# Kernel optimization log

Measured on AMD Instinct MI355X. Metric: run time of the kernel, lower is better.

## Reference

```python
import jax, jax.numpy as jnp
import numpy as np

M, K, N = 8192, 4096, 4096

def setup_inputs() -> dict:
    key = jax.random.key(0)
    k1, k2, k3, k4 = jax.random.split(key, 4)
    x = jax.random.normal(k1, (M, K), dtype=jnp.float32)
    # pre-quantized int8 weights [K, N] and per-output-channel scales [N]
    weight_q = jax.random.randint(k2, (K, N), -128, 128, dtype=jnp.int32).astype(jnp.int8)
    weight_scale = (jax.random.uniform(k3, (N,), dtype=jnp.float32) * 0.01 + 1e-4)
    bias = jax.random.normal(k4, (N,), dtype=jnp.float32) * 0.02
    return {"x": x, "weight_q": weight_q, "weight_scale": weight_scale, "bias": bias}

def reference(x, weight_q, weight_scale, bias):
    # dynamic per-row int8 quantization of activations
    max_vals = jnp.max(jnp.abs(x), axis=-1, keepdims=True)          # [M, 1]
    a_scale = jnp.maximum(max_vals / 127.0, 1e-8)                    # [M, 1]
    x_q = jnp.clip(jnp.round(x / a_scale), -128, 127).astype(jnp.int8)
    c = jnp.matmul(x_q.astype(jnp.float32), weight_q.astype(jnp.float32))  # [M, N]
    # dequantize: per-row activation scale * per-column weight scale
    c = c * a_scale * weight_scale[None, :]
    out = c.astype(x.dtype) + bias
    return out
```

## Files before the change

### kernel.cpp

```cpp
#include <hip/hip_runtime.h>


typedef int int32x4 __attribute__((ext_vector_type(4)));

#define TILE_BM 128
#define TILE_BN 128
#define TILE_BK 64

__device__ __forceinline__ void async_copy16(const void* g, void* l) {
    __builtin_amdgcn_global_load_lds(
        (const __attribute__((address_space(1))) unsigned int*)g,
        (__attribute__((address_space(3))) unsigned int*)l,
        16, 0, 0);
}

__device__ __forceinline__ int quant1(float x, float s) {
    float q = rintf(x / s);
    q = fminf(127.0f, fmaxf(-128.0f, q));
    return (int)q;
}

__global__ __launch_bounds__(256) void quant_kernel(
    const float* __restrict__ x, signed char* __restrict__ xq,
    float* __restrict__ ascale, int K)
{
    const int row = blockIdx.x;
    const int t = threadIdx.x;
    const float4* xr4 = (const float4*)(x + (size_t)row * K);

    float4 v[4];
    float mx = 0.0f;
#pragma unroll
    for (int i = 0; i < 4; ++i) {
        v[i] = xr4[t * 4 + i];
        mx = fmaxf(mx, fmaxf(fmaxf(fabsf(v[i].x), fabsf(v[i].y)),
                             fmaxf(fabsf(v[i].z), fabsf(v[i].w))));
    }
#pragma unroll
    for (int off = 32; off > 0; off >>= 1)
        mx = fmaxf(mx, __shfl_xor(mx, off, 64));
    __shared__ float wmax[4];
    if ((t & 63) == 0) wmax[t >> 6] = mx;
    __syncthreads();
    mx = fmaxf(fmaxf(wmax[0], wmax[1]), fmaxf(wmax[2], wmax[3]));

    const float s = fmaxf(mx / 127.0f, 1e-8f);
    if (t == 0) ascale[row] = s;

    int out[4];
#pragma unroll
    for (int i = 0; i < 4; ++i) {
        const int b0 = quant1(v[i].x, s);
        const int b1 = quant1(v[i].y, s);
        const int b2 = quant1(v[i].z, s);
        const int b3 = quant1(v[i].w, s);
        out[i] = (b0 & 255) | ((b1 & 255) << 8) | ((b2 & 255) << 16) | ((b3 & 255) << 24);
    }
    *(int32x4*)(xq + (size_t)row * K + t * 16) = *(const int32x4*)out;
}

__global__ __launch_bounds__(256) void transpose_pack_kernel(
    const int* __restrict__ Bq, signed char* __restrict__ Bt, int K, int N)
{
    __shared__ int lds[64 * 17];
    const int t = threadIdx.x;
    const int n0 = blockIdx.x * 64;
    const int k0 = blockIdx.y * 64;

    const int r = t >> 4;
    const int ncol = (t & 15) * 4;

    const int* src = Bq + (size_t)(k0 + 4 * r) * N + n0 + ncol;
    const int4 u0 = *(const int4*)(src);
    const int4 u1 = *(const int4*)(src + N);
    const int4 u2 = *(const int4*)(src + 2 * (size_t)N);
    const int4 u3 = *(const int4*)(src + 3 * (size_t)N);

    lds[(ncol + 0) * 17 + r] = (u0.x & 255) | ((u1.x & 255) << 8) | ((u2.x & 255) << 16) | ((u3.x & 255) << 24);
    lds[(ncol + 1) * 17 + r] = (u0.y & 255) | ((u1.y & 255) << 8) | ((u2.y & 255) << 16) | ((u3.y & 255) << 24);
    lds[(ncol + 2) * 17 + r] = (u0.z & 255) | ((u1.z & 255) << 8) | ((u2.z & 255) << 16) | ((u3.z & 255) << 24);
    lds[(ncol + 3) * 17 + r] = (u0.w & 255) | ((u1.w & 255) << 8) | ((u2.w & 255) << 16) | ((u3.w & 255) << 24);
    __syncthreads();

    const int nl = t >> 2, ch = t & 3;
    int o[4];
#pragma unroll
    for (int i = 0; i < 4; ++i) o[i] = lds[nl * 17 + ch * 4 + i];
    *(int32x4*)(Bt + (size_t)(n0 + nl) * K + k0 + ch * 16) = *(const int32x4*)o;
}

__global__ __launch_bounds__(256, 2) void gemm_i8_kernel(
    const signed char* __restrict__ Aq, const signed char* __restrict__ Bt,
    const float* __restrict__ ascale, const float* __restrict__ wscale,
    const float* __restrict__ bias, float* __restrict__ C,
    int M, int N, int K)
{
    __shared__ __align__(16) signed char As[TILE_BM * TILE_BK];
    __shared__ __align__(16) signed char Bs[TILE_BN * TILE_BK];

    const int t = threadIdx.x;
    const int lane = t & 63;
    const int w = t >> 6;
    const int wr = w >> 1, wc = w & 1;

    const int m0 = blockIdx.y * TILE_BM;
    const int n0 = blockIdx.x * TILE_BN;

    const int srow = t >> 2;
    const int schunk = (t & 3) * 16;
    const signed char* gA0 = Aq + (size_t)(m0 + srow) * K + schunk;
    const signed char* gA1 = gA0 + (size_t)64 * K;
    const signed char* gB0 = Bt + (size_t)(n0 + srow) * K + schunk;
    const signed char* gB1 = gB0 + (size_t)64 * K;
    signed char* lA0 = As + t * 16;
    signed char* lA1 = lA0 + 4096;
    signed char* lB0 = Bs + t * 16;
    signed char* lB1 = lB0 + 4096;

    const int kb16 = (lane >> 4) * 16;
    const int ml = lane & 15;
    const signed char* fA = As + (wr * 64 + ml) * TILE_BK + kb16;
    const signed char* fB = Bs + (wc * 64 + ml) * TILE_BK + kb16;

    int32x4 acc[4][4] = {};

    for (int k0 = 0; k0 < K; k0 += TILE_BK) {
        async_copy16(gA0 + k0, lA0);
        async_copy16(gA1 + k0, lA1);
        async_copy16(gB0 + k0, lB0);
        async_copy16(gB1 + k0, lB1);
        __syncthreads();

        int32x4 af[4], bf[4];
#pragma unroll
        for (int i = 0; i < 4; ++i) {
            af[i] = *(const int32x4*)(fA + i * 16 * TILE_BK);
            bf[i] = *(const int32x4*)(fB + i * 16 * TILE_BK);
        }
#pragma unroll
        for (int i = 0; i < 4; ++i)
#pragma unroll
            for (int j = 0; j < 4; ++j)
                acc[i][j] = __builtin_amdgcn_mfma_i32_16x16x64_i8(af[i], bf[j], acc[i][j], 0, 0, 0);
        __syncthreads();
    }

    const int colb = n0 + wc * 64 + ml;
    const int rowb = m0 + wr * 64 + (lane >> 4) * 4;
#pragma unroll
    for (int j = 0; j < 4; ++j) {
        const int col = colb + j * 16;
        const float ws = wscale[col];
        const float bs = bias[col];
#pragma unroll
        for (int i = 0; i < 4; ++i) {
            const int row = rowb + i * 16;
            float* cp = C + (size_t)row * N + col;
#pragma unroll
            for (int r = 0; r < 4; ++r) {
                cp[(size_t)r * N] = ((float)acc[i][j][r] * ascale[row + r]) * ws + bs;
            }
        }
    }
}

extern "C" void kernel_launch(void* const* d_in, const int* in_sizes, int n_in,
                              void* d_out, int out_size, void* d_ws, size_t ws_size,
                              hipStream_t stream) {
    const float* x      = (const float*)d_in[0];
    const int*   wq     = (const int*)d_in[1];
    const float* wscale = (const float*)d_in[2];
    const float* bias   = (const float*)d_in[3];
    float* out          = (float*)d_out;

    const int N = in_sizes[2];
    const int K = in_sizes[1] / N;
    const int M = in_sizes[0] / K;

    char* ws = (char*)d_ws;
    signed char* xq = (signed char*)ws;
    signed char* bt = (signed char*)(ws + (size_t)M * K);
    float* ascale   = (float*)(ws + (size_t)M * K + (size_t)N * K);

    quant_kernel<<<M, 256, 0, stream>>>(x, xq, ascale, K);
    transpose_pack_kernel<<<dim3(N / 64, K / 64), 256, 0, stream>>>(wq, bt, K, N);
    gemm_i8_kernel<<<dim3(N / TILE_BN, M / TILE_BM), 256, 0, stream>>>(
        xq, bt, ascale, wscale, bias, out, M, N, K);
}
```

Measured before the change: 427.5 us.

## Fuse prep kernels, switch GEMM to 32x32 MFMA with BK=128 and swizzled LDS

The quantization and weight transpose/pack kernels are merged into one launch whose blocks branch on index, which removes one launch and lets the two jobs overlap. The GEMM K-tile doubles to 128, the 16x16x64 int8 MFMA is replaced with 32x32x32 in a 2x2 per-wave layout, and an XOR swizzle is applied to LDS chunks to avoid bank conflicts. The goal is fewer barriers per K, fewer LDS fragment reads per MFMA, and a vectorized ascale load in the epilogue. LDS use doubles to 32KB per block while launch bounds ask for 3 blocks per CU, which could raise register pressure.

```diff
diff --git a/kernel.cpp b/kernel.cpp
--- a/kernel.cpp
+++ b/kernel.cpp
@@ -1,11 +1,13 @@
 #include <hip/hip_runtime.h>
 
 
-typedef int int32x4 __attribute__((ext_vector_type(4)));
+typedef int   int32x4  __attribute__((ext_vector_type(4)));
+typedef int   int32x16 __attribute__((ext_vector_type(16)));
+typedef float floatx4  __attribute__((ext_vector_type(4)));
 
-#define TILE_BM 128
-#define TILE_BN 128
-#define TILE_BK 64
+#define BM 128
+#define BN 128
+#define BK 128
 
 __device__ __forceinline__ void async_copy16(const void* g, void* l) {
     __builtin_amdgcn_global_load_lds(
@@ -20,145 +22,153 @@
     return (int)q;
 }
 
-__global__ __launch_bounds__(256) void quant_kernel(
-    const float* __restrict__ x, signed char* __restrict__ xq,
-    float* __restrict__ ascale, int K)
+__global__ __launch_bounds__(256) void prep_kernel(
+    const float* __restrict__ x, const int* __restrict__ Bq,
+    signed char* __restrict__ xq, signed char* __restrict__ Bt,
+    float* __restrict__ ascale, int M, int K, int N)
 {
-    const int row = blockIdx.x;
+    __shared__ __align__(16) int shmem[64 * 17];
     const int t = threadIdx.x;
-    const float4* xr4 = (const float4*)(x + (size_t)row * K);
+    const int b = (int)blockIdx.x;
 
-    float4 v[4];
-    float mx = 0.0f;
+    if (b < M) {
+        const int row = b;
+        const float4* xr4 = (const float4*)(x + (size_t)row * K);
+        float4 v[4];
+        float mx = 0.0f;
 #pragma unroll
-    for (int i = 0; i < 4; ++i) {
-        v[i] = xr4[t * 4 + i];
-        mx = fmaxf(mx, fmaxf(fmaxf(fabsf(v[i].x), fabsf(v[i].y)),
-                             fmaxf(fabsf(v[i].z), fabsf(v[i].w))));
+        for (int i = 0; i < 4; ++i) {
+            v[i] = xr4[t * 4 + i];
+            mx = fmaxf(mx, fmaxf(fmaxf(fabsf(v[i].x), fabsf(v[i].y)),
+                                 fmaxf(fabsf(v[i].z), fabsf(v[i].w))));
+        }
+#pragma unroll
+        for (int off = 32; off > 0; off >>= 1)
+            mx = fmaxf(mx, __shfl_xor(mx, off, 64));
+        float* wmax = (float*)shmem;
+        if ((t & 63) == 0) wmax[t >> 6] = mx;
+        __syncthreads();
+        mx = fmaxf(fmaxf(wmax[0], wmax[1]), fmaxf(wmax[2], wmax[3]));
+
+        const float s = fmaxf(mx / 127.0f, 1e-8f);
+        if (t == 0) ascale[row] = s;
+
+        int out[4];
+#pragma unroll
+        for (int i = 0; i < 4; ++i) {
+            const int b0 = quant1(v[i].x, s);
+            const int b1 = quant1(v[i].y, s);
+            const int b2 = quant1(v[i].z, s);
+            const int b3 = quant1(v[i].w, s);
+            out[i] = (b0 & 255) | ((b1 & 255) << 8) | ((b2 & 255) << 16) | ((b3 & 255) << 24);
+        }
+        *(int32x4*)(xq + (size_t)row * K + t * 16) = *(const int32x4*)out;
+    } else {
+        const int tile = b - M;
+        const int tiles_n = N >> 6;
+        const int n0 = (tile % tiles_n) * 64;
+        const int k0 = (tile / tiles_n) * 64;
+
+        const int r = t >> 4;
+        const int ncol = (t & 15) * 4;
+
+        const int* src = Bq + (size_t)(k0 + 4 * r) * N + n0 + ncol;
+        const int4 u0 = *(const int4*)(src);
+        const int4 u1 = *(const int4*)(src + N);
+        const int4 u2 = *(const int4*)(src + 2 * (size_t)N);
+        const int4 u3 = *(const int4*)(src + 3 * (size_t)N);
+
+        shmem[(ncol + 0) * 17 + r] = (u0.x & 255) | ((u1.x & 255) << 8) | ((u2.x & 255) << 16) | ((u3.x & 255) << 24);
+        shmem[(ncol + 1) * 17 + r] = (u0.y & 255) | ((u1.y & 255) << 8) | ((u2.y & 255) << 16) | ((u3.y & 255) << 24);
+        shmem[(ncol + 2) * 17 + r] = (u0.z & 255) | ((u1.z & 255) << 8) | ((u2.z & 255) << 16) | ((u3.z & 255) << 24);
+        shmem[(ncol + 3) * 17 + r] = (u0.w & 255) | ((u1.w & 255) << 8) | ((u2.w & 255) << 16) | ((u3.w & 255) << 24);
+        __syncthreads();
+
+        const int nl = t >> 2, ch = t & 3;
+        int o[4];
+#pragma unroll
+        for (int i = 0; i < 4; ++i) o[i] = shmem[nl * 17 + ch * 4 + i];
+        *(int32x4*)(Bt + (size_t)(n0 + nl) * K + k0 + ch * 16) = *(const int32x4*)o;
     }
-#pragma unroll
-    for (int off = 32; off > 0; off >>= 1)
-        mx = fmaxf(mx, __shfl_xor(mx, off, 64));
-    __shared__ float wmax[4];
-    if ((t & 63) == 0) wmax[t >> 6] = mx;
-    __syncthreads();
-    mx = fmaxf(fmaxf(wmax[0], wmax[1]), fmaxf(wmax[2], wmax[3]));
-
-    const float s = fmaxf(mx / 127.0f, 1e-8f);
-    if (t == 0) ascale[row] = s;
-
-    int out[4];
-#pragma unroll
-    for (int i = 0; i < 4; ++i) {
-        const int b0 = quant1(v[i].x, s);
-        const int b1 = quant1(v[i].y, s);
-        const int b2 = quant1(v[i].z, s);
-        const int b3 = quant1(v[i].w, s);
-        out[i] = (b0 & 255) | ((b1 & 255) << 8) | ((b2 & 255) << 16) | ((b3 & 255) << 24);
-    }
-    *(int32x4*)(xq + (size_t)row * K + t * 16) = *(const int32x4*)out;
 }
 
-__global__ __launch_bounds__(256) void transpose_pack_kernel(
-    const int* __restrict__ Bq, signed char* __restrict__ Bt, int K, int N)
-{
-    __shared__ int lds[64 * 17];
-    const int t = threadIdx.x;
-    const int n0 = blockIdx.x * 64;
-    const int k0 = blockIdx.y * 64;
-
-    const int r = t >> 4;
-    const int ncol = (t & 15) * 4;
-
-    const int* src = Bq + (size_t)(k0 + 4 * r) * N + n0 + ncol;
-    const int4 u0 = *(const int4*)(src);
-    const int4 u1 = *(const int4*)(src + N);
-    const int4 u2 = *(const int4*)(src + 2 * (size_t)N);
-    const int4 u3 = *(const int4*)(src + 3 * (size_t)N);
-
-    lds[(ncol + 0) * 17 + r] = (u0.x & 255) | ((u1.x & 255) << 8) | ((u2.x & 255) << 16) | ((u3.x & 255) << 24);
-    lds[(ncol + 1) * 17 + r] = (u0.y & 255) | ((u1.y & 255) << 8) | ((u2.y & 255) << 16) | ((u3.y & 255) << 24);
-    lds[(ncol + 2) * 17 + r] = (u0.z & 255) | ((u1.z & 255) << 8) | ((u2.z & 255) << 16) | ((u3.z & 255) << 24);
-    lds[(ncol + 3) * 17 + r] = (u0.w & 255) | ((u1.w & 255) << 8) | ((u2.w & 255) << 16) | ((u3.w & 255) << 24);
-    __syncthreads();
-
-    const int nl = t >> 2, ch = t & 3;
-    int o[4];
-#pragma unroll
-    for (int i = 0; i < 4; ++i) o[i] = lds[nl * 17 + ch * 4 + i];
-    *(int32x4*)(Bt + (size_t)(n0 + nl) * K + k0 + ch * 16) = *(const int32x4*)o;
-}
-
-__global__ __launch_bounds__(256, 2) void gemm_i8_kernel(
+__global__ __launch_bounds__(256, 3) void gemm_i8_kernel(
     const signed char* __restrict__ Aq, const signed char* __restrict__ Bt,
     const float* __restrict__ ascale, const float* __restrict__ wscale,
     const float* __restrict__ bias, float* __restrict__ C,
     int M, int N, int K)
 {
-    __shared__ __align__(16) signed char As[TILE_BM * TILE_BK];
-    __shared__ __align__(16) signed char Bs[TILE_BN * TILE_BK];
+    __shared__ __align__(16) signed char As[BM * BK];
+    __shared__ __align__(16) signed char Bs[BN * BK];
 
     const int t = threadIdx.x;
     const int lane = t & 63;
     const int w = t >> 6;
     const int wr = w >> 1, wc = w & 1;
 
-    const int m0 = blockIdx.y * TILE_BM;
-    const int n0 = blockIdx.x * TILE_BN;
+    const int m0 = blockIdx.y * BM;
+    const int n0 = blockIdx.x * BN;
 
-    const int srow = t >> 2;
-    const int schunk = (t & 3) * 16;
-    const signed char* gA0 = Aq + (size_t)(m0 + srow) * K + schunk;
-    const signed char* gA1 = gA0 + (size_t)64 * K;
-    const signed char* gB0 = Bt + (size_t)(n0 + srow) * K + schunk;
-    const signed char* gB1 = gB0 + (size_t)64 * K;
-    signed char* lA0 = As + t * 16;
-    signed char* lA1 = lA0 + 4096;
-    signed char* lB0 = Bs + t * 16;
-    signed char* lB1 = lB0 + 4096;
+    const int srow = t >> 3;
+    const int schunk = ((t & 7) ^ (srow & 7)) * 16;
+    const signed char* gA = Aq + (size_t)(m0 + srow) * K + schunk;
+    const signed char* gB = Bt + (size_t)(n0 + srow) * K + schunk;
+    signed char* lA = As + t * 16;
+    signed char* lB = Bs + t * 16;
 
-    const int kb16 = (lane >> 4) * 16;
-    const int ml = lane & 15;
-    const signed char* fA = As + (wr * 64 + ml) * TILE_BK + kb16;
-    const signed char* fB = Bs + (wc * 64 + ml) * TILE_BK + kb16;
+    const int ml = lane & 31;
+    const int half = lane >> 5;
+    const int sw = ml & 7;
+    const signed char* fA0 = As + (wr * 64 + ml) * BK;
+    const signed char* fA1 = fA0 + 32 * BK;
+    const signed char* fB0 = Bs + (wc * 64 + ml) * BK;
+    const signed char* fB1 = fB0 + 32 * BK;
 
-    int32x4 acc[4][4] = {};
+    int32x16 acc[2][2] = {};
 
-    for (int k0 = 0; k0 < K; k0 += TILE_BK) {
-        async_copy16(gA0 + k0, lA0);
-        async_copy16(gA1 + k0, lA1);
-        async_copy16(gB0 + k0, lB0);
-        async_copy16(gB1 + k0, lB1);
+    for (int k0 = 0; k0 < K; k0 += BK) {
+#pragma unroll
+        for (int r = 0; r < 8; ++r)
+            async_copy16(gA + k0 + (size_t)r * 32 * K, lA + r * 4096);
+#pragma unroll
+        for (int r = 0; r < 8; ++r)
+            async_copy16(gB + k0 + (size_t)r * 32 * K, lB + r * 4096);
         __syncthreads();
 
-        int32x4 af[4], bf[4];
 #pragma unroll
-        for (int i = 0; i < 4; ++i) {
-            af[i] = *(const int32x4*)(fA + i * 16 * TILE_BK);
-            bf[i] = *(const int32x4*)(fB + i * 16 * TILE_BK);
+        for (int kk = 0; kk < 4; ++kk) {
+            const int chunk = kk * 2 + half;
+            const int off = ((chunk ^ sw) * 16);
+            int32x4 a0 = *(const int32x4*)(fA0 + off);
+            int32x4 a1 = *(const int32x4*)(fA1 + off);
+            int32x4 b0 = *(const int32x4*)(fB0 + off);
+            int32x4 b1 = *(const int32x4*)(fB1 + off);
+            acc[0][0] = __builtin_amdgcn_mfma_i32_32x32x32_i8(a0, b0, acc[0][0], 0, 0, 0);
+            acc[0][1] = __builtin_amdgcn_mfma_i32_32x32x32_i8(a0, b1, acc[0][1], 0, 0, 0);
+            acc[1][0] = __builtin_amdgcn_mfma_i32_32x32x32_i8(a1, b0, acc[1][0], 0, 0, 0);
+            acc[1][1] = __builtin_amdgcn_mfma_i32_32x32x32_i8(a1, b1, acc[1][1], 0, 0, 0);
         }
-#pragma unroll
-        for (int i = 0; i < 4; ++i)
-#pragma unroll
-            for (int j = 0; j < 4; ++j)
-                acc[i][j] = __builtin_amdgcn_mfma_i32_16x16x64_i8(af[i], bf[j], acc[i][j], 0, 0, 0);
         __syncthreads();
     }
 
-    const int colb = n0 + wc * 64 + ml;
-    const int rowb = m0 + wr * 64 + (lane >> 4) * 4;
+    const int rowoff = 4 * half;
 #pragma unroll
-    for (int j = 0; j < 4; ++j) {
-        const int col = colb + j * 16;
+    for (int j = 0; j < 2; ++j) {
+        const int col = n0 + wc * 64 + j * 32 + ml;
         const float ws = wscale[col];
         const float bs = bias[col];
 #pragma unroll
-        for (int i = 0; i < 4; ++i) {
-            const int row = rowb + i * 16;
-            float* cp = C + (size_t)row * N + col;
+        for (int i = 0; i < 2; ++i) {
+            const int rbase = m0 + wr * 64 + i * 32 + rowoff;
 #pragma unroll
-            for (int r = 0; r < 4; ++r) {
-                cp[(size_t)r * N] = ((float)acc[i][j][r] * ascale[row + r]) * ws + bs;
+            for (int g = 0; g < 4; ++g) {
+                const int rg = rbase + 8 * g;
+                const floatx4 as4 = *(const floatx4*)(ascale + rg);
+                float* cp = C + (size_t)rg * N + col;
+#pragma unroll
+                for (int rr = 0; rr < 4; ++rr) {
+                    cp[(size_t)rr * N] = ((float)acc[i][j][g * 4 + rr] * as4[rr]) * ws + bs;
+                }
             }
         }
     }
@@ -182,8 +192,8 @@
     signed char* bt = (signed char*)(ws + (size_t)M * K);
     float* ascale   = (float*)(ws + (size_t)M * K + (size_t)N * K);
 
-    quant_kernel<<<M, 256, 0, stream>>>(x, xq, ascale, K);
-    transpose_pack_kernel<<<dim3(N / 64, K / 64), 256, 0, stream>>>(wq, bt, K, N);
-    gemm_i8_kernel<<<dim3(N / TILE_BN, M / TILE_BM), 256, 0, stream>>>(
+    const int prep_blocks = M + (N / 64) * (K / 64);
+    prep_kernel<<<prep_blocks, 256, 0, stream>>>(x, wq, xq, bt, ascale, M, K, N);
+    gemm_i8_kernel<<<dim3(N / BN, M / BM), 256, 0, stream>>>(
         xq, bt, ascale, wscale, bias, out, M, N, K);
 }
```

Measured after the change: 443.9 us. 1.04x slower.
